# Performance work log

Hardware: AMD Instinct MI355X
Metric: run time of the kernel (lower is better)

The kernel has to match this reference:

```python
import jax, jax.numpy as jnp
import numpy as np

B, S, D, H = 2, 2048, 1024, 16
HW = D // H  # head width = 64
MASK_FILL = -100000000.0


def setup_inputs() -> dict:
    key0 = jax.random.key(0)
    ks = jax.random.split(key0, 12)
    inp = {
        "query": jax.random.normal(ks[0], (B, S, D), jnp.float32),
        "key": jax.random.normal(ks[1], (B, S, D), jnp.float32),
        "value": jax.random.normal(ks[2], (B, S, D), jnp.float32),
        # bool mask, True masks; broadcasts over batch and heads
        "mask": jax.random.randint(ks[3], (S, S), 0, 2).astype(jnp.bool_),
        # per-head projection kernels: (heads, head_width, d_in)
        "Wq": jax.random.normal(ks[4], (H, HW, D), jnp.float32) * 0.02,
        "bq": jnp.zeros((H, HW), jnp.float32),
        "Wk": jax.random.normal(ks[5], (H, HW, D), jnp.float32) * 0.02,
        "bk": jnp.zeros((H, HW), jnp.float32),
        "Wv": jax.random.normal(ks[6], (H, HW, D), jnp.float32) * 0.02,
        "bv": jnp.zeros((H, HW), jnp.float32),
        # collapse projector: contracts (heads, head_width) -> d_output
        "Wo": jax.random.normal(ks[7], (D, H, HW), jnp.float32) * 0.02,
        "bo": jnp.zeros((D,), jnp.float32),
    }
    return inp


def reference(query, key, value, mask, Wq, bq, Wk, bk, Wv, bv, Wo, bo):
    # head projections -> (b, h, s, w)
    q = jnp.einsum("bsd,hwd->bhsw", query, Wq) + bq[:, None, :]
    k = jnp.einsum("btd,hwd->bhtw", key, Wk) + bk[:, None, :]
    v = jnp.einsum("btd,hwd->bhtw", value, Wv) + bv[:, None, :]
    # unscaled logits, masked_fill, softmax (matches original exactly)
    logits = jnp.einsum("bhsw,bhtw->bhst", q, k)
    logits = jnp.where(mask, MASK_FILL, logits)
    score = jax.nn.softmax(logits, axis=-1)
    # NOTE: original divides AV output by sqrt(head_width) AFTER softmax
    attn = jnp.einsum("bhst,bhtw->bhsw", score, v) / jnp.sqrt(jnp.float32(HW))
    # collapse heads -> (b, s, d_output)
    out = jnp.einsum("bhsw,ohw->bso", attn, Wo) + bo
    return out
```

## Files before the change

### kernel.cpp

```cpp
#include <hip/hip_runtime.h>
#include <math.h>

#define S_LEN   2048
#define D_MODEL 1024
#define N_HEADS 16
#define HEAD_W  64
#define BATCH   2
#define MROWS   (BATCH * S_LEN)
#define MASK_FILL -100000000.0f
#define LOG2E 1.4426950408889634f

typedef __attribute__((ext_vector_type(8))) short bf16x8;
typedef __attribute__((ext_vector_type(4))) float f32x4;
typedef unsigned short u16;
typedef unsigned int   u32;
typedef unsigned long long u64;

__device__ __forceinline__ u16 f2bf(float f) {
    u32 u = __float_as_uint(f);
    return (u16)((u + 0x7fffu + ((u >> 16) & 1u)) >> 16);
}

__device__ __forceinline__ void gld_lds16(const void* gp, void* lp) {
    __builtin_amdgcn_global_load_lds(
        (const __attribute__((address_space(1))) u32*)gp,
        (__attribute__((address_space(3))) u32*)lp, 16, 0, 0);
}

__global__ void detect_mask_kernel(const unsigned char* __restrict__ mask,
                                   int* __restrict__ flag) {
    __shared__ int cnt;
    if (threadIdx.x == 0) cnt = 0;
    __syncthreads();
    int c = 0;
    for (int i = threadIdx.x; i < 16384; i += 256)
        if ((i & 3) != 0 && mask[i] != 0) c++;
    if (c) atomicAdd(&cnt, c);
    __syncthreads();
    if (threadIdx.x == 0) *flag = (cnt == 0) ? 1 : 0;
}

__global__ void mask_bits_kernel(const void* __restrict__ mask,
                                 const int* __restrict__ flag,
                                 u64* __restrict__ bits) {
    const int isInt = *flag;
    const int stride = gridDim.x * 256;
    for (int i = blockIdx.x * 256 + threadIdx.x; i < S_LEN * S_LEN; i += stride) {
        bool m = isInt ? (((const int*)mask)[i] != 0)
                       : (((const unsigned char*)mask)[i] != 0);
        u64 b = __ballot(m);
        if ((i & 63) == 0) bits[i >> 6] = b;
    }
}

struct CvtJobs {
    const float* src[7];
    u16* dst[7];
    int n[7];
};
__global__ void cvt_bf16_kernel(CvtJobs j) {
    const int t = blockIdx.y;
    const float* s = j.src[t];
    u16* d = j.dst[t];
    const int n = j.n[t];
    int i = (blockIdx.x * 256 + threadIdx.x) * 4;
    if (i < n) {
        float4 v = *(const float4*)(s + i);
        ushort4 o;
        o.x = f2bf(v.x); o.y = f2bf(v.y); o.z = f2bf(v.z); o.w = f2bf(v.w);
        *(ushort4*)(d + i) = o;
    }
}

__device__ __forceinline__ void gemm_core_bf16(const u16* __restrict__ A,
                                               const u16* __restrict__ Bt,
                                               int m0, int n0, f32x4 acc[4][4]) {
    __shared__ u16 As[2][4096];
    __shared__ u16 Bs[2][4096];
    const int tid = threadIdx.x;
    const int wv = tid >> 6, ln = tid & 63;
    const int lane16 = ln & 15, quad = ln >> 4;
    const int wr = (wv >> 1) * 64, wc = (wv & 1) * 64;
    const u16* A0 = A + (size_t)(m0 + ln) * D_MODEL + wv * 8;
    const u16* A1 = A + (size_t)(m0 + 64 + ln) * D_MODEL + wv * 8;
    const u16* B0 = Bt + (size_t)(n0 + ln) * D_MODEL + wv * 8;
    const u16* B1 = Bt + (size_t)(n0 + 64 + ln) * D_MODEL + wv * 8;

    gld_lds16(A0, &As[0][wv * 1024]);
    gld_lds16(A1, &As[0][wv * 1024 + 512]);
    gld_lds16(B0, &Bs[0][wv * 1024]);
    gld_lds16(B1, &Bs[0][wv * 1024 + 512]);

    for (int kt = 0; kt < D_MODEL / 32; ++kt) {
        const int buf = kt & 1;
        __syncthreads();
        if (kt < D_MODEL / 32 - 1) {
            const int ko = (kt + 1) * 32;
            gld_lds16(A0 + ko, &As[buf ^ 1][wv * 1024]);
            gld_lds16(A1 + ko, &As[buf ^ 1][wv * 1024 + 512]);
            gld_lds16(B0 + ko, &Bs[buf ^ 1][wv * 1024]);
            gld_lds16(B1 + ko, &Bs[buf ^ 1][wv * 1024 + 512]);
        }
        bf16x8 af[4], bfv[4];
#pragma unroll
        for (int mt = 0; mt < 4; ++mt)
            af[mt] = *(const bf16x8*)&As[buf][quad * 1024 + (wr + mt * 16 + lane16) * 8];
#pragma unroll
        for (int nt = 0; nt < 4; ++nt)
            bfv[nt] = *(const bf16x8*)&Bs[buf][quad * 1024 + (wc + nt * 16 + lane16) * 8];
#pragma unroll
        for (int mt = 0; mt < 4; ++mt)
#pragma unroll
            for (int nt = 0; nt < 4; ++nt)
                acc[mt][nt] = __builtin_amdgcn_mfma_f32_16x16x32_bf16(
                    af[mt], bfv[nt], acc[mt][nt], 0, 0, 0);
    }
}

__global__ __launch_bounds__(256, 2) void qkv_gemm_kernel(
    const u16* __restrict__ xq, const u16* __restrict__ xk, const u16* __restrict__ xv,
    const u16* __restrict__ wq, const u16* __restrict__ wk, const u16* __restrict__ wv,
    const float* __restrict__ bq, const float* __restrict__ bk, const float* __restrict__ bv,
    u16* __restrict__ qb, u16* __restrict__ kb, u16* __restrict__ vbt) {
    const u16* A; const u16* Bt; const float* bias;
    const int z = blockIdx.z;
    if (z == 0)      { A = xq; Bt = wq; bias = bq; }
    else if (z == 1) { A = xk; Bt = wk; bias = bk; }
    else             { A = xv; Bt = wv; bias = bv; }
    f32x4 acc[4][4] = {};
    const int m0 = blockIdx.y * 128, n0 = blockIdx.x * 128;
    gemm_core_bf16(A, Bt, m0, n0, acc);

    const int tid = threadIdx.x;
    const int wvi = tid >> 6, ln = tid & 63;
    const int lane16 = ln & 15, quad = ln >> 4;
    const int wr = (wvi >> 1) * 64, wc = (wvi & 1) * 64;
    const float scale = (z == 0) ? LOG2E : 1.0f;
#pragma unroll
    for (int nt = 0; nt < 4; ++nt) {
        const int n = n0 + wc + nt * 16 + lane16;
        const float bb = bias[n];
        const int h = n >> 6, w = n & 63;
#pragma unroll
        for (int mt = 0; mt < 4; ++mt) {
#pragma unroll
            for (int r = 0; r < 4; ++r) {
                const int m = m0 + wr + mt * 16 + quad * 4 + r;
                const int bidx = m >> 11, s = m & 2047;
                const u16 o = f2bf((acc[mt][nt][r] + bb) * scale);
                if (z == 0)
                    qb[((size_t)((bidx * N_HEADS + h) * S_LEN + s)) * HEAD_W + w] = o;
                else if (z == 1)
                    kb[((size_t)((bidx * N_HEADS + h) * S_LEN + s)) * HEAD_W + w] = o;
                else
                    vbt[((size_t)(bidx * N_HEADS + h) * HEAD_W + w) * S_LEN + s] = o;
            }
        }
    }
}

__global__ __launch_bounds__(256, 2) void out_gemm_kernel(
    const u16* __restrict__ ab, const u16* __restrict__ wo,
    const float* __restrict__ bo, float* __restrict__ out) {
    f32x4 acc[4][4] = {};
    const int m0 = blockIdx.y * 128, n0 = blockIdx.x * 128;
    gemm_core_bf16(ab, wo, m0, n0, acc);
    const int tid = threadIdx.x;
    const int wvi = tid >> 6, ln = tid & 63;
    const int lane16 = ln & 15, quad = ln >> 4;
    const int wr = (wvi >> 1) * 64, wc = (wvi & 1) * 64;
#pragma unroll
    for (int nt = 0; nt < 4; ++nt) {
        const int n = n0 + wc + nt * 16 + lane16;
        const float bb = bo[n];
#pragma unroll
        for (int mt = 0; mt < 4; ++mt)
#pragma unroll
            for (int r = 0; r < 4; ++r) {
                const int m = m0 + wr + mt * 16 + quad * 4 + r;
                out[(size_t)m * D_MODEL + n] = acc[mt][nt][r] + bb;
            }
    }
}

__global__ __launch_bounds__(256, 2) void attn_kernel(
    const u16* __restrict__ qbuf, const u16* __restrict__ kbuf,
    const u16* __restrict__ vbt, const u64* __restrict__ mbits,
    u16* __restrict__ abuf) {
    __shared__ u16 Ks[2][4096];
    __shared__ u16 Vt[2][4096];
    __shared__ u16 Ps[4][32 * 72];
    const int tid = threadIdx.x;
    const int wv = tid >> 6, ln = tid & 63;
    const int lane16 = ln & 15, quad = ln >> 4;
    const int s_blk = blockIdx.x * 128;
    const int h = blockIdx.y, b = blockIdx.z;
    const size_t hb = ((size_t)(b * N_HEADS + h)) * S_LEN * HEAD_W;
    const u16* Qg = qbuf + hb;
    const u16* Kg = kbuf + hb;
    const u16* Vg = vbt + hb;

    bf16x8 qa[2][2];
#pragma unroll
    for (int mt = 0; mt < 2; ++mt)
#pragma unroll
        for (int kk = 0; kk < 2; ++kk)
            qa[mt][kk] = *(const bf16x8*)(Qg +
                (size_t)(s_blk + wv * 32 + mt * 16 + lane16) * HEAD_W + kk * 32 + quad * 8);

    const size_t mrow0 = (size_t)(s_blk + wv * 32 + lane16) * 32;
    const size_t mrow1 = (size_t)(s_blk + wv * 32 + 16 + lane16) * 32;
    u64 mwCur0 = mbits[mrow0], mwCur1 = mbits[mrow1];
    u64 mwNx0 = 0, mwNx1 = 0;

    {
        const int i0 = 2 * wv, i1 = 2 * wv + 1;
        gld_lds16(Kg + (size_t)ln * HEAD_W + i0 * 8, &Ks[0][i0 * 512]);
        gld_lds16(Kg + (size_t)ln * HEAD_W + i1 * 8, &Ks[0][i1 * 512]);
        gld_lds16(Vg + (size_t)ln * S_LEN + i0 * 8, &Vt[0][i0 * 512]);
        gld_lds16(Vg + (size_t)ln * S_LEN + i1 * 8, &Vt[0][i1 * 512]);
    }

    f32x4 oacc[2][4] = {};
    float lsum[2] = {0.0f, 0.0f};

    for (int c = 0; c < S_LEN / 64; ++c) {
        const int buf = c & 1;
        __syncthreads();
        if (c < S_LEN / 64 - 1) {
            const int t1 = (c + 1) * 64;
            const int i0 = 2 * wv, i1 = 2 * wv + 1;
            gld_lds16(Kg + (size_t)(t1 + ln) * HEAD_W + i0 * 8, &Ks[buf ^ 1][i0 * 512]);
            gld_lds16(Kg + (size_t)(t1 + ln) * HEAD_W + i1 * 8, &Ks[buf ^ 1][i1 * 512]);
            gld_lds16(Vg + (size_t)ln * S_LEN + t1 + i0 * 8, &Vt[buf ^ 1][i0 * 512]);
            gld_lds16(Vg + (size_t)ln * S_LEN + t1 + i1 * 8, &Vt[buf ^ 1][i1 * 512]);
            mwNx0 = mbits[mrow0 + c + 1];
            mwNx1 = mbits[mrow1 + c + 1];
        }

        f32x4 st[4][2] = {};
#pragma unroll
        for (int kk = 0; kk < 2; ++kk)
#pragma unroll
            for (int ntT = 0; ntT < 4; ++ntT) {
                bf16x8 kf = *(const bf16x8*)&Ks[buf][(kk * 4 + quad) * 512 + (ntT * 16 + lane16) * 8];
#pragma unroll
                for (int mt = 0; mt < 2; ++mt)
                    st[ntT][mt] = __builtin_amdgcn_mfma_f32_16x16x32_bf16(
                        kf, qa[mt][kk], st[ntT][mt], 0, 0, 0);
            }

#pragma unroll
        for (int mt = 0; mt < 2; ++mt) {
            const u64 mw = mt ? mwCur1 : mwCur0;
            float ls = 0.0f;
#pragma unroll
            for (int ntT = 0; ntT < 4; ++ntT) {
                const u32 nib = (u32)(mw >> (ntT * 16 + quad * 4)) & 15u;
                float p0 = exp2f(st[ntT][mt][0]); if (nib & 1u) p0 = 0.0f;
                float p1 = exp2f(st[ntT][mt][1]); if (nib & 2u) p1 = 0.0f;
                float p2 = exp2f(st[ntT][mt][2]); if (nib & 4u) p2 = 0.0f;
                float p3 = exp2f(st[ntT][mt][3]); if (nib & 8u) p3 = 0.0f;
                ls += (p0 + p1) + (p2 + p3);
                uint2 pk;
                pk.x = __builtin_amdgcn_perm(__float_as_uint(p1) + 0x8000u,
                                             __float_as_uint(p0) + 0x8000u, 0x07060302u);
                pk.y = __builtin_amdgcn_perm(__float_as_uint(p3) + 0x8000u,
                                             __float_as_uint(p2) + 0x8000u, 0x07060302u);
                *(uint2*)&Ps[wv][(mt * 16 + lane16) * 72 + ntT * 16 + quad * 4] = pk;
            }
            lsum[mt] += ls;
        }

        bf16x8 pf[2][2];
#pragma unroll
        for (int mt = 0; mt < 2; ++mt)
#pragma unroll
            for (int kk = 0; kk < 2; ++kk)
                pf[mt][kk] = *(const bf16x8*)&Ps[wv][(mt * 16 + lane16) * 72 + kk * 32 + quad * 8];
#pragma unroll
        for (int kk = 0; kk < 2; ++kk)
#pragma unroll
            for (int ntw = 0; ntw < 4; ++ntw) {
                bf16x8 vf = *(const bf16x8*)&Vt[buf][(kk * 4 + quad) * 512 + (ntw * 16 + lane16) * 8];
#pragma unroll
                for (int mt = 0; mt < 2; ++mt)
                    oacc[mt][ntw] = __builtin_amdgcn_mfma_f32_16x16x32_bf16(
                        pf[mt][kk], vf, oacc[mt][ntw], 0, 0, 0);
            }
        mwCur0 = mwNx0; mwCur1 = mwNx1;
    }

#pragma unroll
    for (int mt = 0; mt < 2; ++mt) {
        float lm = lsum[mt];
        lm += __shfl_xor(lm, 16);
        lm += __shfl_xor(lm, 32);
#pragma unroll
        for (int r = 0; r < 4; ++r) {
            const float lr = __shfl(lm, (ln & 48) | (quad * 4 + r));
            const float inv = 0.125f / lr;
            const int s = s_blk + wv * 32 + mt * 16 + quad * 4 + r;
            u16* dst = abuf + ((size_t)(b * S_LEN + s)) * D_MODEL + h * HEAD_W;
#pragma unroll
            for (int ntw = 0; ntw < 4; ++ntw)
                dst[ntw * 16 + lane16] = f2bf(oacc[mt][ntw][r] * inv);
        }
    }
}

extern "C" void kernel_launch(void* const* d_in, const int* in_sizes, int n_in,
                              void* d_out, int out_size, void* d_ws, size_t ws_size,
                              hipStream_t stream) {
    const float* query = (const float*)d_in[0];
    const float* key   = (const float*)d_in[1];
    const float* value = (const float*)d_in[2];
    const void*  mask  = d_in[3];
    const float* Wq = (const float*)d_in[4];
    const float* bq = (const float*)d_in[5];
    const float* Wk = (const float*)d_in[6];
    const float* bk = (const float*)d_in[7];
    const float* Wv = (const float*)d_in[8];
    const float* bv = (const float*)d_in[9];
    const float* Wo = (const float*)d_in[10];
    const float* bo = (const float*)d_in[11];
    float* out = (float*)d_out;

    char* ws = (char*)d_ws;
    size_t off = 0;
    auto alloc = [&](size_t bytes) -> void* {
        void* p = ws + off;
        off += (bytes + 255) & ~(size_t)255;
        return p;
    };
    const size_t NACT = (size_t)MROWS * D_MODEL;
    const size_t NW   = (size_t)D_MODEL * D_MODEL;
    int* flag = (int*)alloc(4);
    u64* bits = (u64*)alloc((size_t)S_LEN * (S_LEN / 64) * 8);
    u16* xq  = (u16*)alloc(NACT * 2);
    u16* xk  = (u16*)alloc(NACT * 2);
    u16* xv  = (u16*)alloc(NACT * 2);
    u16* wqb = (u16*)alloc(NW * 2);
    u16* wkb = (u16*)alloc(NW * 2);
    u16* wvb = (u16*)alloc(NW * 2);
    u16* wob = (u16*)alloc(NW * 2);
    u16* qb  = (u16*)alloc(NACT * 2);
    u16* kb  = (u16*)alloc(NACT * 2);
    u16* vbt = (u16*)alloc(NACT * 2);
    u16* ab  = (u16*)alloc(NACT * 2);

    detect_mask_kernel<<<1, 256, 0, stream>>>((const unsigned char*)mask, flag);
    mask_bits_kernel<<<2048, 256, 0, stream>>>(mask, flag, bits);

    CvtJobs j;
    j.src[0] = query; j.dst[0] = xq;  j.n[0] = (int)NACT;
    j.src[1] = key;   j.dst[1] = xk;  j.n[1] = (int)NACT;
    j.src[2] = value; j.dst[2] = xv;  j.n[2] = (int)NACT;
    j.src[3] = Wq;    j.dst[3] = wqb; j.n[3] = (int)NW;
    j.src[4] = Wk;    j.dst[4] = wkb; j.n[4] = (int)NW;
    j.src[5] = Wv;    j.dst[5] = wvb; j.n[5] = (int)NW;
    j.src[6] = Wo;    j.dst[6] = wob; j.n[6] = (int)NW;
    cvt_bf16_kernel<<<dim3(NACT / 1024, 7), 256, 0, stream>>>(j);

    qkv_gemm_kernel<<<dim3(D_MODEL / 128, MROWS / 128, 3), 256, 0, stream>>>(
        xq, xk, xv, wqb, wkb, wvb, bq, bk, bv, qb, kb, vbt);
    attn_kernel<<<dim3(S_LEN / 128, N_HEADS, BATCH), 256, 0, stream>>>(
        qb, kb, vbt, bits, ab);
    out_gemm_kernel<<<dim3(D_MODEL / 128, MROWS / 128), 256, 0, stream>>>(
        ab, wob, bo, out);
}
```

Measured before the change: 333.4 us.

## Split attention over key halves, add V transpose and combine kernels

Attention now splits the key dimension into two halves, doubling grid size. Each half writes unnormalized fp32 partial outputs and row sums, and a new combine kernel sums them and normalizes to bf16. The V projection is written row-major and transposed by a separate LDS tile kernel instead of a strided scatter in the GEMM epilogue. Mask detection is merged into the bit-packing kernel, and the workspace is laid out with aliasing. The aim is better occupancy and coalesced stores, at the cost of extra launches and fp32 partial traffic.

```diff
diff --git a/kernel.cpp b/kernel.cpp
--- a/kernel.cpp
+++ b/kernel.cpp
@@ -27,29 +27,23 @@
         (__attribute__((address_space(3))) u32*)lp, 16, 0, 0);
 }
 
-__global__ void detect_mask_kernel(const unsigned char* __restrict__ mask,
-                                   int* __restrict__ flag) {
-    __shared__ int cnt;
-    if (threadIdx.x == 0) cnt = 0;
+__global__ __launch_bounds__(256) void mask_bits_kernel(
+    const unsigned char* __restrict__ mask, u64* __restrict__ bits) {
+    __shared__ int isByte;
+    if (threadIdx.x == 0) isByte = 0;
     __syncthreads();
-    int c = 0;
-    for (int i = threadIdx.x; i < 16384; i += 256)
-        if ((i & 3) != 0 && mask[i] != 0) c++;
-    if (c) atomicAdd(&cnt, c);
+    const int e0 = blockIdx.x * 2048;
+    const uint2 v = ((const uint2*)(mask + e0))[threadIdx.x];
+    if (((v.x | v.y) & 0xFFFFFF00u) != 0u) isByte = 1;
     __syncthreads();
-    if (threadIdx.x == 0) *flag = (cnt == 0) ? 1 : 0;
-}
-
-__global__ void mask_bits_kernel(const void* __restrict__ mask,
-                                 const int* __restrict__ flag,
-                                 u64* __restrict__ bits) {
-    const int isInt = *flag;
-    const int stride = gridDim.x * 256;
-    for (int i = blockIdx.x * 256 + threadIdx.x; i < S_LEN * S_LEN; i += stride) {
-        bool m = isInt ? (((const int*)mask)[i] != 0)
-                       : (((const unsigned char*)mask)[i] != 0);
-        u64 b = __ballot(m);
-        if ((i & 63) == 0) bits[i >> 6] = b;
+    const int ib = isByte;
+    const int* mi = (const int*)mask;
+#pragma unroll
+    for (int j = 0; j < 8; ++j) {
+        const int e = e0 + j * 256 + threadIdx.x;
+        const bool m = ib ? (mask[e] != 0) : (mi[e] != 0);
+        const u64 bl = __ballot(m);
+        if ((e & 63) == 0) bits[e >> 6] = bl;
     }
 }
 
@@ -121,12 +115,12 @@
     const u16* __restrict__ xq, const u16* __restrict__ xk, const u16* __restrict__ xv,
     const u16* __restrict__ wq, const u16* __restrict__ wk, const u16* __restrict__ wv,
     const float* __restrict__ bq, const float* __restrict__ bk, const float* __restrict__ bv,
-    u16* __restrict__ qb, u16* __restrict__ kb, u16* __restrict__ vbt) {
-    const u16* A; const u16* Bt; const float* bias;
+    u16* __restrict__ qb, u16* __restrict__ kb, u16* __restrict__ vtmp) {
+    const u16* A; const u16* Bt; const float* bias; u16* outp;
     const int z = blockIdx.z;
-    if (z == 0)      { A = xq; Bt = wq; bias = bq; }
-    else if (z == 1) { A = xk; Bt = wk; bias = bk; }
-    else             { A = xv; Bt = wv; bias = bv; }
+    if (z == 0)      { A = xq; Bt = wq; bias = bq; outp = qb; }
+    else if (z == 1) { A = xk; Bt = wk; bias = bk; outp = kb; }
+    else             { A = xv; Bt = wv; bias = bv; outp = vtmp; }
     f32x4 acc[4][4] = {};
     const int m0 = blockIdx.y * 128, n0 = blockIdx.x * 128;
     gemm_core_bf16(A, Bt, m0, n0, acc);
@@ -142,21 +136,35 @@
         const float bb = bias[n];
         const int h = n >> 6, w = n & 63;
 #pragma unroll
-        for (int mt = 0; mt < 4; ++mt) {
+        for (int mt = 0; mt < 4; ++mt)
 #pragma unroll
             for (int r = 0; r < 4; ++r) {
                 const int m = m0 + wr + mt * 16 + quad * 4 + r;
                 const int bidx = m >> 11, s = m & 2047;
-                const u16 o = f2bf((acc[mt][nt][r] + bb) * scale);
-                if (z == 0)
-                    qb[((size_t)((bidx * N_HEADS + h) * S_LEN + s)) * HEAD_W + w] = o;
-                else if (z == 1)
-                    kb[((size_t)((bidx * N_HEADS + h) * S_LEN + s)) * HEAD_W + w] = o;
-                else
-                    vbt[((size_t)(bidx * N_HEADS + h) * HEAD_W + w) * S_LEN + s] = o;
+                outp[((size_t)((bidx * N_HEADS + h) * S_LEN + s)) * HEAD_W + w] =
+                    f2bf((acc[mt][nt][r] + bb) * scale);
             }
-        }
-    }
+    }
+}
+
+__global__ __launch_bounds__(256) void vtrans_kernel(
+    const u16* __restrict__ vtmp, u16* __restrict__ vbt) {
+    __shared__ u16 T[64][72];
+    const int tid = threadIdx.x;
+    const int bh = blockIdx.y;
+    const int s0 = blockIdx.x * 64;
+    const int row = tid >> 2, seg = (tid & 3) * 16;
+    const u16* src = vtmp + ((size_t)bh * S_LEN + s0 + row) * HEAD_W + seg;
+    uint4 a = *(const uint4*)src;
+    uint4 b2 = *(const uint4*)(src + 8);
+    u16 tmp[16];
+    *(uint4*)tmp = a; *(uint4*)(tmp + 8) = b2;
+#pragma unroll
+    for (int j = 0; j < 16; ++j) T[seg + j][row] = tmp[j];
+    __syncthreads();
+    u16* dst = vbt + ((size_t)bh * HEAD_W + row) * S_LEN + s0 + seg;
+    *(uint4*)dst       = *(const uint4*)&T[row][seg];
+    *(uint4*)(dst + 8) = *(const uint4*)&T[row][seg + 8];
 }
 
 __global__ __launch_bounds__(256, 2) void out_gemm_kernel(
@@ -186,7 +194,7 @@
 __global__ __launch_bounds__(256, 2) void attn_kernel(
     const u16* __restrict__ qbuf, const u16* __restrict__ kbuf,
     const u16* __restrict__ vbt, const u64* __restrict__ mbits,
-    u16* __restrict__ abuf) {
+    float* __restrict__ Opart, float* __restrict__ lpart) {
     __shared__ u16 Ks[2][4096];
     __shared__ u16 Vt[2][4096];
     __shared__ u16 Ps[4][32 * 72];
@@ -194,7 +202,9 @@
     const int wv = tid >> 6, ln = tid & 63;
     const int lane16 = ln & 15, quad = ln >> 4;
     const int s_blk = blockIdx.x * 128;
-    const int h = blockIdx.y, b = blockIdx.z;
+    const int h = blockIdx.y;
+    const int b = blockIdx.z >> 1, hf = blockIdx.z & 1;
+    const int c0 = hf * 16;
     const size_t hb = ((size_t)(b * N_HEADS + h)) * S_LEN * HEAD_W;
     const u16* Qg = qbuf + hb;
     const u16* Kg = kbuf + hb;
@@ -210,24 +220,26 @@
 
     const size_t mrow0 = (size_t)(s_blk + wv * 32 + lane16) * 32;
     const size_t mrow1 = (size_t)(s_blk + wv * 32 + 16 + lane16) * 32;
-    u64 mwCur0 = mbits[mrow0], mwCur1 = mbits[mrow1];
+    u64 mwCur0 = mbits[mrow0 + c0], mwCur1 = mbits[mrow1 + c0];
     u64 mwNx0 = 0, mwNx1 = 0;
 
     {
+        const int t0g = c0 * 64;
         const int i0 = 2 * wv, i1 = 2 * wv + 1;
-        gld_lds16(Kg + (size_t)ln * HEAD_W + i0 * 8, &Ks[0][i0 * 512]);
-        gld_lds16(Kg + (size_t)ln * HEAD_W + i1 * 8, &Ks[0][i1 * 512]);
-        gld_lds16(Vg + (size_t)ln * S_LEN + i0 * 8, &Vt[0][i0 * 512]);
-        gld_lds16(Vg + (size_t)ln * S_LEN + i1 * 8, &Vt[0][i1 * 512]);
+        gld_lds16(Kg + (size_t)(t0g + ln) * HEAD_W + i0 * 8, &Ks[0][i0 * 512]);
+        gld_lds16(Kg + (size_t)(t0g + ln) * HEAD_W + i1 * 8, &Ks[0][i1 * 512]);
+        gld_lds16(Vg + (size_t)ln * S_LEN + t0g + i0 * 8, &Vt[0][i0 * 512]);
+        gld_lds16(Vg + (size_t)ln * S_LEN + t0g + i1 * 8, &Vt[0][i1 * 512]);
     }
 
     f32x4 oacc[2][4] = {};
     float lsum[2] = {0.0f, 0.0f};
 
-    for (int c = 0; c < S_LEN / 64; ++c) {
-        const int buf = c & 1;
+    for (int ci = 0; ci < 16; ++ci) {
+        const int c = c0 + ci;
+        const int buf = ci & 1;
         __syncthreads();
-        if (c < S_LEN / 64 - 1) {
+        if (ci < 15) {
             const int t1 = (c + 1) * 64;
             const int i0 = 2 * wv, i1 = 2 * wv + 1;
             gld_lds16(Kg + (size_t)(t1 + ln) * HEAD_W + i0 * 8, &Ks[buf ^ 1][i0 * 512]);
@@ -291,22 +303,44 @@
         mwCur0 = mwNx0; mwCur1 = mwNx1;
     }
 
+    float* OpB = Opart + ((size_t)(hf * 4096 + b * 2048)) * 1024;
 #pragma unroll
     for (int mt = 0; mt < 2; ++mt) {
+#pragma unroll
+        for (int r = 0; r < 4; ++r) {
+            const int s = s_blk + wv * 32 + mt * 16 + quad * 4 + r;
+            float* dst = OpB + (size_t)s * 1024 + h * 64;
+#pragma unroll
+            for (int ntw = 0; ntw < 4; ++ntw)
+                dst[ntw * 16 + lane16] = oacc[mt][ntw][r];
+        }
         float lm = lsum[mt];
         lm += __shfl_xor(lm, 16);
         lm += __shfl_xor(lm, 32);
-#pragma unroll
-        for (int r = 0; r < 4; ++r) {
-            const float lr = __shfl(lm, (ln & 48) | (quad * 4 + r));
-            const float inv = 0.125f / lr;
-            const int s = s_blk + wv * 32 + mt * 16 + quad * 4 + r;
-            u16* dst = abuf + ((size_t)(b * S_LEN + s)) * D_MODEL + h * HEAD_W;
-#pragma unroll
-            for (int ntw = 0; ntw < 4; ++ntw)
-                dst[ntw * 16 + lane16] = f2bf(oacc[mt][ntw][r] * inv);
+        if (quad == 0) {
+            const int srow = s_blk + wv * 32 + mt * 16 + lane16;
+            lpart[(size_t)(hf * 4096 + b * 2048 + srow) * 16 + h] = lm;
         }
     }
+}
+
+__global__ __launch_bounds__(256) void combine_kernel(
+    const float* __restrict__ Op, const float* __restrict__ lp,
+    u16* __restrict__ ab) {
+    const int idx4 = blockIdx.x * 256 + threadIdx.x;
+    const int row = idx4 >> 8;
+    const int d = (idx4 & 255) * 4;
+    const int h = d >> 6;
+    const float l = lp[(size_t)row * 16 + h] + lp[(size_t)(4096 + row) * 16 + h];
+    const float inv = 0.125f / l;
+    float4 a = *(const float4*)(Op + (size_t)row * 1024 + d);
+    float4 b = *(const float4*)(Op + (size_t)(4096 + row) * 1024 + d);
+    ushort4 o;
+    o.x = f2bf((a.x + b.x) * inv);
+    o.y = f2bf((a.y + b.y) * inv);
+    o.z = f2bf((a.z + b.z) * inv);
+    o.w = f2bf((a.w + b.w) * inv);
+    *(ushort4*)(ab + (size_t)row * 1024 + d) = o;
 }
 
 extern "C" void kernel_launch(void* const* d_in, const int* in_sizes, int n_in,
@@ -327,30 +361,28 @@
     float* out = (float*)d_out;
 
     char* ws = (char*)d_ws;
-    size_t off = 0;
-    auto alloc = [&](size_t bytes) -> void* {
-        void* p = ws + off;
-        off += (bytes + 255) & ~(size_t)255;
-        return p;
-    };
+    const size_t MB = 1024 * 1024;
+    u64* bits = (u64*)ws;
+    u16* wob  = (u16*)(ws + 1 * MB);
+    u16* qb   = (u16*)(ws + 3 * MB);
+    u16* kb   = (u16*)(ws + 11 * MB);
+    u16* vbt  = (u16*)(ws + 19 * MB);
+    char* uA = ws + 27 * MB;
+    u16* xq   = (u16*)(uA);
+    u16* xk   = (u16*)(uA + 8 * MB);
+    u16* xv   = (u16*)(uA + 16 * MB);
+    u16* wqb  = (u16*)(uA + 24 * MB);
+    u16* wkb  = (u16*)(uA + 26 * MB);
+    u16* wvb  = (u16*)(uA + 28 * MB);
+    u16* vtmp = (u16*)(uA + 30 * MB);
+    float* Opart = (float*)(uA);
+    float* lpart = (float*)(uA + 32 * MB);
+    u16* ab = qb;
+
     const size_t NACT = (size_t)MROWS * D_MODEL;
     const size_t NW   = (size_t)D_MODEL * D_MODEL;
-    int* flag = (int*)alloc(4);
-    u64* bits = (u64*)alloc((size_t)S_LEN * (S_LEN / 64) * 8);
-    u16* xq  = (u16*)alloc(NACT * 2);
-    u16* xk  = (u16*)alloc(NACT * 2);
-    u16* xv  = (u16*)alloc(NACT * 2);
-    u16* wqb = (u16*)alloc(NW * 2);
-    u16* wkb = (u16*)alloc(NW * 2);
-    u16* wvb = (u16*)alloc(NW * 2);
-    u16* wob = (u16*)alloc(NW * 2);
-    u16* qb  = (u16*)alloc(NACT * 2);
-    u16* kb  = (u16*)alloc(NACT * 2);
-    u16* vbt = (u16*)alloc(NACT * 2);
-    u16* ab  = (u16*)alloc(NACT * 2);
-
-    detect_mask_kernel<<<1, 256, 0, stream>>>((const unsigned char*)mask, flag);
-    mask_bits_kernel<<<2048, 256, 0, stream>>>(mask, flag, bits);
+
+    mask_bits_kernel<<<2048, 256, 0, stream>>>((const unsigned char*)mask, bits);
 
     CvtJobs j;
     j.src[0] = query; j.dst[0] = xq;  j.n[0] = (int)NACT;
@@ -363,9 +395,11 @@
     cvt_bf16_kernel<<<dim3(NACT / 1024, 7), 256, 0, stream>>>(j);
 
     qkv_gemm_kernel<<<dim3(D_MODEL / 128, MROWS / 128, 3), 256, 0, stream>>>(
-        xq, xk, xv, wqb, wkb, wvb, bq, bk, bv, qb, kb, vbt);
-    attn_kernel<<<dim3(S_LEN / 128, N_HEADS, BATCH), 256, 0, stream>>>(
-        qb, kb, vbt, bits, ab);
+        xq, xk, xv, wqb, wkb, wvb, bq, bk, bv, qb, kb, vtmp);
+    vtrans_kernel<<<dim3(S_LEN / 64, BATCH * N_HEADS), 256, 0, stream>>>(vtmp, vbt);
+    attn_kernel<<<dim3(S_LEN / 128, N_HEADS, BATCH * 2), 256, 0, stream>>>(
+        qb, kb, vbt, bits, Opart, lpart);
+    combine_kernel<<<4096, 256, 0, stream>>>(Opart, lpart, ab);
     out_gemm_kernel<<<dim3(D_MODEL / 128, MROWS / 128), 256, 0, stream>>>(
         ab, wob, bo, out);
 }
```

New measurement: 313.8 us. 5.9% less time.
